# Performance work log

Measured on AMD Instinct MI355X. Metric: run time of the kernel, lower is better.

Reference implementation:

```python
import jax, jax.numpy as jnp
import numpy as np

DIM = 256
HEADS = 4
HEAD_DIM = DIM // HEADS          # 64
KEY_DIM = HEAD_DIM // 2          # 32 (attn_ratio=0.5)
HIDDEN = DIM + 2 * KEY_DIM * HEADS  # 512
B, H, W = 2, 64, 64
EPS = 1e-5


def _conv2d(x, w, groups=1, pad=0):
    return jax.lax.conv_general_dilated(
        x, w, window_strides=(1, 1), padding=[(pad, pad), (pad, pad)],
        dimension_numbers=('NCHW', 'OIHW', 'NCHW'), feature_group_count=groups)


def _bn(x, g, b, m, v):
    scale = g / jnp.sqrt(v + EPS)
    return x * scale[None, :, None, None] + (b - m * scale)[None, :, None, None]


def setup_inputs() -> dict:
    key = jax.random.key(0)
    ks = jax.random.split(key, 16)
    d = {
        'x': jax.random.normal(ks[0], (B, DIM, H, W), jnp.float32),
        'qkv_w': jax.random.normal(ks[1], (HIDDEN, DIM, 1, 1), jnp.float32) * 0.05,
        'qkv_g': jax.random.uniform(ks[2], (HIDDEN,), jnp.float32, 0.5, 1.5),
        'qkv_b': jax.random.normal(ks[3], (HIDDEN,), jnp.float32) * 0.1,
        'qkv_m': jax.random.normal(ks[4], (HIDDEN,), jnp.float32) * 0.1,
        'qkv_v': jax.random.uniform(ks[5], (HIDDEN,), jnp.float32, 0.5, 1.5),
        'proj_w': jax.random.normal(ks[6], (DIM, DIM, 1, 1), jnp.float32) * 0.05,
        'proj_g': jax.random.uniform(ks[7], (DIM,), jnp.float32, 0.5, 1.5),
        'proj_b': jax.random.normal(ks[8], (DIM,), jnp.float32) * 0.1,
        'proj_m': jax.random.normal(ks[9], (DIM,), jnp.float32) * 0.1,
        'proj_v': jax.random.uniform(ks[10], (DIM,), jnp.float32, 0.5, 1.5),
        'pe_w': jax.random.normal(ks[11], (DIM, 1, 3, 3), jnp.float32) * 0.1,
        'pe_g': jax.random.uniform(ks[12], (DIM,), jnp.float32, 0.5, 1.5),
        'pe_b': jax.random.normal(ks[13], (DIM,), jnp.float32) * 0.1,
        'pe_m': jax.random.normal(ks[14], (DIM,), jnp.float32) * 0.1,
        'pe_v': jax.random.uniform(ks[15], (DIM,), jnp.float32, 0.5, 1.5),
    }
    return d


def reference(x, qkv_w, qkv_g, qkv_b, qkv_m, qkv_v,
              proj_w, proj_g, proj_b, proj_m, proj_v,
              pe_w, pe_g, pe_b, pe_m, pe_v):
    b, c, h, w = x.shape
    n = h * w
    scale = KEY_DIM ** -0.5

    qkv = _bn(_conv2d(x, qkv_w), qkv_g, qkv_b, qkv_m, qkv_v)  # [b, hidden, h, w]
    qkv = qkv.reshape(b, HEADS, 2 * KEY_DIM + HEAD_DIM, n)
    q = qkv[:, :, :KEY_DIM]                       # [b, heads, key_dim, n]
    k = qkv[:, :, KEY_DIM:2 * KEY_DIM]            # [b, heads, key_dim, n]
    v = qkv[:, :, 2 * KEY_DIM:]                   # [b, heads, head_dim, n]

    # attn[b,h,i,j] = sum_d q[b,h,d,i] * k[b,h,d,j] * scale; softmax over j
    attn = jnp.einsum('bhdi,bhdj->bhij', q, k) * scale
    attn = jax.nn.softmax(attn, axis=-1)

    # y = v @ attn^T : out[b,h,d,i] = sum_j v[b,h,d,j] * attn[b,h,i,j]
    y = jnp.einsum('bhdj,bhij->bhdi', v, attn).reshape(b, c, h, w)

    pe = _bn(_conv2d(v.reshape(b, c, h, w), pe_w, groups=c, pad=1),
             pe_g, pe_b, pe_m, pe_v)
    y = y + pe
    return _bn(_conv2d(y, proj_w), proj_g, proj_b, proj_m, proj_v)
```

## Files before the change

kernel.cpp:

```cpp
#include <hip/hip_runtime.h>
#include <hip/hip_bf16.h>

#define NSP 4096
#define BEPS 1e-5f
#define JSPLIT 4
#define JCHUNK (NSP / JSPLIT)

using short8  = __attribute__((ext_vector_type(8))) short;
using half8   = __attribute__((ext_vector_type(8))) _Float16;
using f32x4   = __attribute__((ext_vector_type(4))) float;
using f32x16  = __attribute__((ext_vector_type(16))) float;

#define SCALE_LOG2E 0.2550348883f

__device__ __forceinline__ float b2f(unsigned short u) {
  return __uint_as_float(((unsigned)u) << 16);
}
__device__ __forceinline__ float b2f_lo(unsigned w) {
  return __uint_as_float(w << 16);
}
__device__ __forceinline__ float b2f_hi(unsigned w) {
  return __uint_as_float(w & 0xffff0000u);
}
__device__ __forceinline__ unsigned short f2b(float x) {
  unsigned u = __float_as_uint(x);
  u += 0x7fffu + ((u >> 16) & 1u);
  return (unsigned short)(u >> 16);
}
__device__ __forceinline__ unsigned pk_bf16(float a, float b) {
  return ((unsigned)f2b(b) << 16) | (unsigned)f2b(a);
}
__device__ __forceinline__ unsigned pk2u(float a, float b) {
  __hip_bfloat162 h = __float22bfloat162_rn(float2{a, b});
  unsigned r;
  __builtin_memcpy(&r, &h, sizeof(r));
  return r;
}
__device__ __forceinline__ unsigned short f2h(float x) {
  _Float16 h = (_Float16)x;
  unsigned short u;
  __builtin_memcpy(&u, &h, sizeof(u));
  return u;
}
__device__ __forceinline__ unsigned pk_h2(float a, float b) {
  return ((unsigned)f2h(b) << 16) | (unsigned)f2h(a);
}

__global__ __launch_bounds__(256) void cast_w_kernel(
    const float* __restrict__ qkv_w, const float* __restrict__ proj_w,
    unsigned short* __restrict__ wqb, unsigned short* __restrict__ wpb)
{
  const int i = blockIdx.x * 256 + threadIdx.x;
  if (i < 131072)       wqb[i] = f2h(qkv_w[i]);
  else                  wpb[i - 131072] = f2b(proj_w[i - 131072]);
}

__global__ __launch_bounds__(256) void transpose_x_kernel(
    const float* __restrict__ x, unsigned short* __restrict__ xT)
{
  const int n0 = blockIdx.x * 64, c0 = blockIdx.y * 64, b = blockIdx.z;
  __shared__ __align__(16) unsigned short tx[64][72];
  const int t = threadIdx.x;
  const int row = t >> 2;
  const int seg = t & 3;
  {
    const float* xp = x + ((size_t)(b * 256 + c0 + row)) * NSP + n0 + seg * 16;
    #pragma unroll
    for (int q4 = 0; q4 < 4; ++q4) {
      const float4 a = *reinterpret_cast<const float4*>(xp + q4 * 4);
      tx[seg * 16 + q4 * 4 + 0][row] = f2h(a.x);
      tx[seg * 16 + q4 * 4 + 1][row] = f2h(a.y);
      tx[seg * 16 + q4 * 4 + 2][row] = f2h(a.z);
      tx[seg * 16 + q4 * 4 + 3][row] = f2h(a.w);
    }
  }
  __syncthreads();
  const int nrow = t >> 2, ch = t & 3;
  unsigned short* op = xT + ((size_t)(b * NSP + n0 + nrow)) * 256 + c0 + ch * 16;
  *reinterpret_cast<float4*>(op)     = *reinterpret_cast<const float4*>(&tx[nrow][ch * 16]);
  *reinterpret_cast<float4*>(op + 8) = *reinterpret_cast<const float4*>(&tx[nrow][ch * 16 + 8]);
}

__global__ __launch_bounds__(256) void qkv_gemm_kernel(
    const unsigned short* __restrict__ xT, const unsigned short* __restrict__ wqb,
    const float* __restrict__ gg, const float* __restrict__ bb,
    const float* __restrict__ mm, const float* __restrict__ vv,
    unsigned short* __restrict__ qb, unsigned short* __restrict__ kb,
    unsigned short* __restrict__ vb)
{
  const int n0 = blockIdx.x * 128;
  const int cotile = blockIdx.y;
  const int b = blockIdx.z;
  const int co0 = cotile * 64;
  const int t = threadIdx.x;
  __shared__ __align__(16) unsigned short wt[64][136];
  __shared__ __align__(16) unsigned short xt[128][136];
  const int lane = t & 63, wave = t >> 6;
  const int m16 = lane & 15, quad = lane >> 4;

  f32x4 acc[8] = {};
  for (int kc = 0; kc < 2; ++kc) {
    if (kc) __syncthreads();
    {
      const unsigned short* wp = wqb + (size_t)(co0 + (t >> 2)) * 256 + kc * 128 + (t & 3) * 32;
      #pragma unroll
      for (int u = 0; u < 4; ++u)
        *reinterpret_cast<float4*>(&wt[t >> 2][(t & 3) * 32 + u * 8]) =
            *reinterpret_cast<const float4*>(wp + u * 8);
      const unsigned short* xp = xT + ((size_t)(b * NSP + n0 + (t >> 1))) * 256 + kc * 128 + (t & 1) * 64;
      #pragma unroll
      for (int u = 0; u < 8; ++u)
        *reinterpret_cast<float4*>(&xt[t >> 1][(t & 1) * 64 + u * 8]) =
            *reinterpret_cast<const float4*>(xp + u * 8);
    }
    __syncthreads();
    if ((cotile & 1) == 0) {
      #pragma unroll
      for (int ks = 0; ks < 4; ++ks) {
        const half8 af = *reinterpret_cast<const half8*>(&wt[wave * 16 + m16][ks * 32 + quad * 8]);
        #pragma unroll
        for (int nt = 0; nt < 8; ++nt) {
          const half8 bf = *reinterpret_cast<const half8*>(&xt[nt * 16 + m16][ks * 32 + quad * 8]);
          acc[nt] = __builtin_amdgcn_mfma_f32_16x16x32_f16(af, bf, acc[nt], 0, 0, 0);
        }
      }
    } else {
      #pragma unroll
      for (int ks = 0; ks < 4; ++ks) {
        const half8 bf = *reinterpret_cast<const half8*>(&wt[wave * 16 + m16][ks * 32 + quad * 8]);
        #pragma unroll
        for (int nt = 0; nt < 8; ++nt) {
          const half8 af = *reinterpret_cast<const half8*>(&xt[nt * 16 + m16][ks * 32 + quad * 8]);
          acc[nt] = __builtin_amdgcn_mfma_f32_16x16x32_f16(af, bf, acc[nt], 0, 0, 0);
        }
      }
    }
  }

  const int head = cotile >> 1;
  const int bh = b * 4 + head;
  if ((cotile & 1) == 0) {
    const int coh = wave * 16 + quad * 4;
    const bool isq = (coh < 32);
    const float fold = isq ? SCALE_LOG2E : 1.0f;
    float sc[4], bi[4];
    #pragma unroll
    for (int r = 0; r < 4; ++r) {
      const int c = co0 + coh + r;
      const float s0 = gg[c] * rsqrtf(vv[c] + BEPS);
      sc[r] = s0 * fold;
      bi[r] = (bb[c] - mm[c] * s0) * fold;
    }
    unsigned short* dst = isq ? qb : kb;
    const int d0 = coh & 31;
    #pragma unroll
    for (int nt = 0; nt < 8; ++nt) {
      const int i = n0 + nt * 16 + m16;
      uint2 pk2;
      pk2.x = pk_h2(acc[nt][0] * sc[0] + bi[0], acc[nt][1] * sc[1] + bi[1]);
      pk2.y = pk_h2(acc[nt][2] * sc[2] + bi[2], acc[nt][3] * sc[3] + bi[3]);
      *reinterpret_cast<uint2*>(dst + ((size_t)bh * NSP + i) * 32 + d0) = pk2;
    }
  } else {
    const int c = co0 + wave * 16 + m16;
    const float sc = gg[c] * rsqrtf(vv[c] + BEPS);
    const float bi = bb[c] - mm[c] * sc;
    const int d = wave * 16 + m16;
    #pragma unroll
    for (int nt = 0; nt < 8; ++nt) {
      const int j = n0 + nt * 16 + quad * 4;
      uint2 pk2;
      pk2.x = pk_bf16(acc[nt][0] * sc + bi, acc[nt][1] * sc + bi);
      pk2.y = pk_bf16(acc[nt][2] * sc + bi, acc[nt][3] * sc + bi);
      *reinterpret_cast<uint2*>(vb + ((size_t)(bh * 64 + d)) * NSP + j) = pk2;
    }
  }
}

__global__ __launch_bounds__(256, 4) void attn_kernel(
    const unsigned short* __restrict__ qb, const unsigned short* __restrict__ kb,
    const unsigned short* __restrict__ vb,
    unsigned short* __restrict__ Opart, float* __restrict__ lpart)
{
  const int i0    = blockIdx.x * 128;
  const int bh    = blockIdx.y;
  const int split = blockIdx.z;
  const int jbase = split * JCHUNK;
  const int t  = threadIdx.x;
  const int lane = t & 63, wave = t >> 6;
  const int l31 = lane & 31, hi = lane >> 5;

  __shared__ __align__(16) unsigned short qs[128][40];
  __shared__ __align__(16) unsigned short ks[64][40];
  __shared__ __align__(16) unsigned short vs[64][72];

  {
    const unsigned short* qp = qb + ((size_t)bh * NSP + i0) * 32;
    const int r = t >> 1, h = t & 1;
    *reinterpret_cast<float4*>(&qs[r][h * 16]) =
        *reinterpret_cast<const float4*>(qp + r * 32 + h * 16);
    *reinterpret_cast<float4*>(&qs[r][h * 16 + 8]) =
        *reinterpret_cast<const float4*>(qp + r * 32 + h * 16 + 8);
  }

  const int srow = t >> 2, schunk = t & 3;
  const unsigned short* kbase = kb + (size_t)bh * NSP * 32;
  const unsigned short* vbase = vb + (size_t)bh * 64 * NSP;

  float4 kreg, vreg0, vreg1;
  kreg  = *reinterpret_cast<const float4*>(kbase + (size_t)(jbase + srow) * 32 + schunk * 8);
  vreg0 = *reinterpret_cast<const float4*>(vbase + (size_t)srow * NSP + jbase + schunk * 16);
  vreg1 = *reinterpret_cast<const float4*>(vbase + (size_t)srow * NSP + jbase + schunk * 16 + 8);

  __syncthreads();
  half8 qfrag[2];
  qfrag[0] = *reinterpret_cast<const half8*>(&qs[wave * 32 + l31][hi * 8]);
  qfrag[1] = *reinterpret_cast<const half8*>(&qs[wave * 32 + l31][16 + hi * 8]);

  *reinterpret_cast<float4*>(&ks[srow][schunk * 8]) = kreg;
  *reinterpret_cast<float4*>(&vs[srow][schunk * 16]) = vreg0;
  *reinterpret_cast<float4*>(&vs[srow][schunk * 16 + 8]) = vreg1;
  __syncthreads();

  float rsum = 0.f;
  f32x16 oacc[2] = {};

  for (int jt0 = 0; jt0 < JCHUNK; jt0 += 64) {
    const bool more = (jt0 + 64) < JCHUNK;
    if (more) {
      const int jn = jbase + jt0 + 64;
      kreg  = *reinterpret_cast<const float4*>(kbase + (size_t)(jn + srow) * 32 + schunk * 8);
      vreg0 = *reinterpret_cast<const float4*>(vbase + (size_t)srow * NSP + jn + schunk * 16);
      vreg1 = *reinterpret_cast<const float4*>(vbase + (size_t)srow * NSP + jn + schunk * 16 + 8);
    }

    half8 kf[2][2];
    #pragma unroll
    for (int jt32 = 0; jt32 < 2; ++jt32) {
      kf[jt32][0] = *reinterpret_cast<const half8*>(&ks[jt32 * 32 + l31][hi * 8]);
      kf[jt32][1] = *reinterpret_cast<const half8*>(&ks[jt32 * 32 + l31][16 + hi * 8]);
    }

    #pragma unroll
    for (int jt32 = 0; jt32 < 2; ++jt32) {
      f32x16 sacc = {};
      sacc = __builtin_amdgcn_mfma_f32_32x32x16_f16(kf[jt32][0], qfrag[0], sacc, 0, 0, 0);
      sacc = __builtin_amdgcn_mfma_f32_32x32x16_f16(kf[jt32][1], qfrag[1], sacc, 0, 0, 0);

      unsigned pk[8];
      #pragma unroll
      for (int c = 0; c < 8; ++c) {
        const float p0 = __builtin_amdgcn_exp2f(sacc[2 * c]);
        const float p1 = __builtin_amdgcn_exp2f(sacc[2 * c + 1]);
        rsum += p0 + p1;
        pk[c] = pk2u(p0, p1);
      }

      #pragma unroll
      for (int kt = 0; kt < 2; ++kt) {
        const unsigned s_a0 = (unsigned)__shfl_xor((int)pk[4 * kt + 0], 32);
        const unsigned s_a1 = (unsigned)__shfl_xor((int)pk[4 * kt + 1], 32);
        const unsigned s_b0 = (unsigned)__shfl_xor((int)pk[4 * kt + 2], 32);
        const unsigned s_b1 = (unsigned)__shfl_xor((int)pk[4 * kt + 3], 32);
        uint4 aw;
        aw.x = hi ? s_b0 : pk[4 * kt + 0];
        aw.y = hi ? s_b1 : pk[4 * kt + 1];
        aw.z = hi ? pk[4 * kt + 2] : s_a0;
        aw.w = hi ? pk[4 * kt + 3] : s_a1;
        short8 af;
        __builtin_memcpy(&af, &aw, 16);
        #pragma unroll
        for (int dt = 0; dt < 2; ++dt) {
          const short8 vf = *reinterpret_cast<const short8*>(
              &vs[dt * 32 + l31][jt32 * 32 + kt * 16 + hi * 8]);
          oacc[dt] = __builtin_amdgcn_mfma_f32_32x32x16_bf16(af, vf, oacc[dt], 0, 0, 0);
        }
      }
    }

    if (more) {
      __syncthreads();
      *reinterpret_cast<float4*>(&ks[srow][schunk * 8]) = kreg;
      *reinterpret_cast<float4*>(&vs[srow][schunk * 16]) = vreg0;
      *reinterpret_cast<float4*>(&vs[srow][schunk * 16 + 8]) = vreg1;
      __syncthreads();
    }
  }

  {
    float rs = rsum;
    rs += __shfl_xor(rs, 32);
    if (hi == 0)
      lpart[((size_t)split * 8 + bh) * NSP + i0 + wave * 32 + l31] = rs;
  }

  #pragma unroll
  for (int dt = 0; dt < 2; ++dt) {
    const int d = dt * 32 + l31;
    #pragma unroll
    for (int R = 0; R < 4; ++R) {
      uint2 pk2;
      pk2.x = pk2u(oacc[dt][4 * R + 0], oacc[dt][4 * R + 1]);
      pk2.y = pk2u(oacc[dt][4 * R + 2], oacc[dt][4 * R + 3]);
      *reinterpret_cast<uint2*>(Opart +
          (((size_t)split * 8 + bh) * 64 + d) * NSP + i0 + wave * 32 + 8 * R + 4 * hi) = pk2;
    }
  }
}

__global__ __launch_bounds__(256) void fuse_kernel(
    const unsigned short* __restrict__ Opart, const float* __restrict__ lpart,
    const unsigned short* __restrict__ vb,
    const float* __restrict__ pw, const float* __restrict__ pg,
    const float* __restrict__ pb, const float* __restrict__ pm,
    const float* __restrict__ pv,
    unsigned short* __restrict__ yT)
{
  const int py = blockIdx.x;
  const int bh = blockIdx.y;
  const int b = bh >> 2, h = bh & 3;
  const int t = threadIdx.x;
  const int d = t >> 2, seg = t & 3;
  __shared__ float lsum[64];
  __shared__ __align__(16) unsigned short yt[64][72];

  if (t < 64) {
    float ls = 0.f;
    #pragma unroll
    for (int s = 0; s < JSPLIT; ++s)
      ls += lpart[((size_t)s * 8 + bh) * NSP + py * 64 + t];
    lsum[t] = ls;
  }
  __syncthreads();

  const int c = h * 64 + d;
  const int i0 = py * 64 + seg * 16;
  float os[16] = {};
  #pragma unroll
  for (int s = 0; s < JSPLIT; ++s) {
    const uint4* op = reinterpret_cast<const uint4*>(
        Opart + (((size_t)s * 8 + bh) * 64 + d) * NSP + i0);
    const uint4 a = op[0], e = op[1];
    os[0]  += b2f_lo(a.x); os[1]  += b2f_hi(a.x);
    os[2]  += b2f_lo(a.y); os[3]  += b2f_hi(a.y);
    os[4]  += b2f_lo(a.z); os[5]  += b2f_hi(a.z);
    os[6]  += b2f_lo(a.w); os[7]  += b2f_hi(a.w);
    os[8]  += b2f_lo(e.x); os[9]  += b2f_hi(e.x);
    os[10] += b2f_lo(e.y); os[11] += b2f_hi(e.y);
    os[12] += b2f_lo(e.z); os[13] += b2f_hi(e.z);
    os[14] += b2f_lo(e.w); os[15] += b2f_hi(e.w);
  }

  float w9[9];
  #pragma unroll
  for (int i = 0; i < 9; ++i) w9[i] = pw[c * 9 + i];
  const float sc = pg[c] * rsqrtf(pv[c] + BEPS);
  const float bi = pb[c] - pm[c] * sc;
  const unsigned short* vrow = vb + ((size_t)(bh * 64 + d)) * NSP;

  float conv[16] = {};
  #pragma unroll
  for (int dy = -1; dy <= 1; ++dy) {
    const int yy = py + dy;
    if (yy < 0 || yy > 63) continue;
    const unsigned short* vr = vrow + yy * 64 + seg * 16;
    float vals[18];
    const uint4 m0 = *reinterpret_cast<const uint4*>(vr);
    const uint4 m1 = *reinterpret_cast<const uint4*>(vr + 8);
    vals[1]  = b2f_lo(m0.x); vals[2]  = b2f_hi(m0.x);
    vals[3]  = b2f_lo(m0.y); vals[4]  = b2f_hi(m0.y);
    vals[5]  = b2f_lo(m0.z); vals[6]  = b2f_hi(m0.z);
    vals[7]  = b2f_lo(m0.w); vals[8]  = b2f_hi(m0.w);
    vals[9]  = b2f_lo(m1.x); vals[10] = b2f_hi(m1.x);
    vals[11] = b2f_lo(m1.y); vals[12] = b2f_hi(m1.y);
    vals[13] = b2f_lo(m1.z); vals[14] = b2f_hi(m1.z);
    vals[15] = b2f_lo(m1.w); vals[16] = b2f_hi(m1.w);
    vals[0]  = (seg > 0) ? b2f_hi(*reinterpret_cast<const unsigned*>(vr - 2)) : 0.f;
    vals[17] = (seg < 3) ? b2f_lo(*reinterpret_cast<const unsigned*>(vr + 16)) : 0.f;
    const float wr0 = w9[(dy + 1) * 3 + 0], wr1 = w9[(dy + 1) * 3 + 1], wr2 = w9[(dy + 1) * 3 + 2];
    #pragma unroll
    for (int u = 0; u < 16; ++u)
      conv[u] += vals[u] * wr0 + vals[u + 1] * wr1 + vals[u + 2] * wr2;
  }

  #pragma unroll
  for (int u = 0; u < 16; ++u) {
    const float yv = os[u] / lsum[seg * 16 + u] + conv[u] * sc + bi;
    yt[seg * 16 + u][d] = f2b(yv);
  }
  __syncthreads();

  const int prow = t >> 2, ch = t & 3;
  unsigned short* op = yT + ((size_t)(b * NSP + py * 64 + prow)) * 256 + h * 64 + ch * 16;
  *reinterpret_cast<float4*>(op)     = *reinterpret_cast<const float4*>(&yt[prow][ch * 16]);
  *reinterpret_cast<float4*>(op + 8) = *reinterpret_cast<const float4*>(&yt[prow][ch * 16 + 8]);
}

__global__ __launch_bounds__(256) void proj_gemm_kernel(
    const unsigned short* __restrict__ yT, const unsigned short* __restrict__ wpb,
    const float* __restrict__ gg, const float* __restrict__ bb,
    const float* __restrict__ mm, const float* __restrict__ vv,
    float* __restrict__ out)
{
  const int n0 = blockIdx.x * 128;
  const int co0 = blockIdx.y * 64;
  const int b = blockIdx.z;
  const int t = threadIdx.x;
  __shared__ __align__(16) unsigned short wt[64][136];
  __shared__ __align__(16) unsigned short yt[128][136];
  const int lane = t & 63, wave = t >> 6;
  const int m16 = lane & 15, quad = lane >> 4;

  f32x4 acc[8] = {};
  for (int kc = 0; kc < 2; ++kc) {
    if (kc) __syncthreads();
    {
      const unsigned short* wp = wpb + (size_t)(co0 + (t >> 2)) * 256 + kc * 128 + (t & 3) * 32;
      #pragma unroll
      for (int u = 0; u < 4; ++u)
        *reinterpret_cast<float4*>(&wt[t >> 2][(t & 3) * 32 + u * 8]) =
            *reinterpret_cast<const float4*>(wp + u * 8);
      const unsigned short* yp = yT + ((size_t)(b * NSP + n0 + (t >> 1))) * 256 + kc * 128 + (t & 1) * 64;
      #pragma unroll
      for (int u = 0; u < 8; ++u)
        *reinterpret_cast<float4*>(&yt[t >> 1][(t & 1) * 64 + u * 8]) =
            *reinterpret_cast<const float4*>(yp + u * 8);
    }
    __syncthreads();
    #pragma unroll
    for (int ks = 0; ks < 4; ++ks) {
      const short8 bf = *reinterpret_cast<const short8*>(&wt[wave * 16 + m16][ks * 32 + quad * 8]);
      #pragma unroll
      for (int nt = 0; nt < 8; ++nt) {
        const short8 af = *reinterpret_cast<const short8*>(&yt[nt * 16 + m16][ks * 32 + quad * 8]);
        acc[nt] = __builtin_amdgcn_mfma_f32_16x16x32_bf16(af, bf, acc[nt], 0, 0, 0);
      }
    }
  }

  const int c = co0 + wave * 16 + m16;
  const float sc = gg[c] * rsqrtf(vv[c] + BEPS);
  const float bi = bb[c] - mm[c] * sc;
  #pragma unroll
  for (int nt = 0; nt < 8; ++nt) {
    const int n = n0 + nt * 16 + quad * 4;
    float4 ov;
    ov.x = acc[nt][0] * sc + bi; ov.y = acc[nt][1] * sc + bi;
    ov.z = acc[nt][2] * sc + bi; ov.w = acc[nt][3] * sc + bi;
    *reinterpret_cast<float4*>(out + ((size_t)(b * 256 + c)) * NSP + n) = ov;
  }
}

extern "C" void kernel_launch(void* const* d_in, const int* in_sizes, int n_in,
                              void* d_out, int out_size, void* d_ws, size_t ws_size,
                              hipStream_t stream)
{
  const float* x      = (const float*)d_in[0];
  const float* qkv_w  = (const float*)d_in[1];
  const float* qkv_g  = (const float*)d_in[2];
  const float* qkv_b  = (const float*)d_in[3];
  const float* qkv_m  = (const float*)d_in[4];
  const float* qkv_v  = (const float*)d_in[5];
  const float* proj_w = (const float*)d_in[6];
  const float* proj_g = (const float*)d_in[7];
  const float* proj_b = (const float*)d_in[8];
  const float* proj_m = (const float*)d_in[9];
  const float* proj_v = (const float*)d_in[10];
  const float* pe_w   = (const float*)d_in[11];
  const float* pe_g   = (const float*)d_in[12];
  const float* pe_b   = (const float*)d_in[13];
  const float* pe_m   = (const float*)d_in[14];
  const float* pe_v   = (const float*)d_in[15];
  float* out = (float*)d_out;

  unsigned short* qb = (unsigned short*)d_ws;
  unsigned short* kb = qb + (size_t)8 * NSP * 32;
  unsigned short* vb = kb + (size_t)8 * NSP * 32;
  unsigned short* Opart = vb + (size_t)8 * 64 * NSP;
  float* lpart = (float*)(Opart + (size_t)JSPLIT * 8 * 64 * NSP);
  unsigned short* xT = (unsigned short*)(lpart + (size_t)JSPLIT * 8 * NSP);
  unsigned short* yT = xT + (size_t)2 * NSP * 256;
  unsigned short* wqb = yT + (size_t)2 * NSP * 256;
  unsigned short* wpb = wqb + (size_t)512 * 256;

  cast_w_kernel<<<dim3(768), 256, 0, stream>>>(qkv_w, proj_w, wqb, wpb);
  transpose_x_kernel<<<dim3(64, 4, 2), 256, 0, stream>>>(x, xT);
  qkv_gemm_kernel<<<dim3(32, 8, 2), 256, 0, stream>>>(xT, wqb, qkv_g, qkv_b, qkv_m, qkv_v,
                                                      qb, kb, vb);
  attn_kernel<<<dim3(32, 8, JSPLIT), 256, 0, stream>>>(qb, kb, vb, Opart, lpart);
  fuse_kernel<<<dim3(64, 8), 256, 0, stream>>>(Opart, lpart, vb,
                                               pe_w, pe_g, pe_b, pe_m, pe_v, yT);
  proj_gemm_kernel<<<dim3(32, 4, 2), 256, 0, stream>>>(yT, wpb, proj_g, proj_b, proj_m, proj_v,
                                                       out);
}
```

Before: 158.6 us.

## Fuse weight cast into transpose, drop attn shuffles, shrink proj tiles

Merges the weight-cast kernel into the x-transpose kernel as an extra grid slice, removing one launch. In attention, Q and K share LDS space, and V is stored with an interleaved layout so each lane's packed P values already match the MFMA operand order. This removes four cross-lane shuffles and selects per inner step. The fuse kernel multiplies by a precomputed reciprocal of the softmax sum instead of dividing. The projection GEMM uses 64-wide spatial tiles to double its block count, at the cost of reloading the weight tile more often.

```diff
diff --git a/kernel.cpp b/kernel.cpp
--- a/kernel.cpp
+++ b/kernel.cpp
@@ -46,21 +46,24 @@
   return ((unsigned)f2h(b) << 16) | (unsigned)f2h(a);
 }
 
-__global__ __launch_bounds__(256) void cast_w_kernel(
+__global__ __launch_bounds__(256) void transpose_x_kernel(
+    const float* __restrict__ x, unsigned short* __restrict__ xT,
     const float* __restrict__ qkv_w, const float* __restrict__ proj_w,
     unsigned short* __restrict__ wqb, unsigned short* __restrict__ wpb)
 {
-  const int i = blockIdx.x * 256 + threadIdx.x;
-  if (i < 131072)       wqb[i] = f2h(qkv_w[i]);
-  else                  wpb[i - 131072] = f2b(proj_w[i - 131072]);
-}
-
-__global__ __launch_bounds__(256) void transpose_x_kernel(
-    const float* __restrict__ x, unsigned short* __restrict__ xT)
-{
+  const int t = threadIdx.x;
+  if (blockIdx.z == 2) {
+    const int tid = (blockIdx.x * 4 + blockIdx.y) * 256 + t;
+    #pragma unroll
+    for (int u = 0; u < 3; ++u) {
+      const int i = tid + u * 65536;
+      if (i < 131072)  wqb[i] = f2h(qkv_w[i]);
+      else             wpb[i - 131072] = f2b(proj_w[i - 131072]);
+    }
+    return;
+  }
   const int n0 = blockIdx.x * 64, c0 = blockIdx.y * 64, b = blockIdx.z;
   __shared__ __align__(16) unsigned short tx[64][72];
-  const int t = threadIdx.x;
   const int row = t >> 2;
   const int seg = t & 3;
   {
@@ -190,9 +193,10 @@
   const int lane = t & 63, wave = t >> 6;
   const int l31 = lane & 31, hi = lane >> 5;
 
-  __shared__ __align__(16) unsigned short qs[128][40];
-  __shared__ __align__(16) unsigned short ks[64][40];
-  __shared__ __align__(16) unsigned short vs[64][72];
+  __shared__ __align__(16) unsigned short smem[7168];
+  unsigned short (*qs)[40] = (unsigned short(*)[40])smem;
+  unsigned short (*ks)[40] = (unsigned short(*)[40])smem;
+  unsigned short (*vs)[72] = (unsigned short(*)[72])(smem + 2560);
 
   {
     const unsigned short* qp = qb + ((size_t)bh * NSP + i0) * 32;
@@ -216,10 +220,18 @@
   half8 qfrag[2];
   qfrag[0] = *reinterpret_cast<const half8*>(&qs[wave * 32 + l31][hi * 8]);
   qfrag[1] = *reinterpret_cast<const half8*>(&qs[wave * 32 + l31][16 + hi * 8]);
+  __syncthreads();
 
   *reinterpret_cast<float4*>(&ks[srow][schunk * 8]) = kreg;
-  *reinterpret_cast<float4*>(&vs[srow][schunk * 16]) = vreg0;
-  *reinterpret_cast<float4*>(&vs[srow][schunk * 16 + 8]) = vreg1;
+  {
+    uint2* vd = reinterpret_cast<uint2*>(&vs[srow][schunk * 16]);
+    const uint2* v0 = reinterpret_cast<const uint2*>(&vreg0);
+    const uint2* v1 = reinterpret_cast<const uint2*>(&vreg1);
+    vd[0] = v0[0];
+    vd[1] = v1[0];
+    vd[2] = v0[1];
+    vd[3] = v1[1];
+  }
   __syncthreads();
 
   float rsum = 0.f;
@@ -258,15 +270,11 @@
 
       #pragma unroll
       for (int kt = 0; kt < 2; ++kt) {
-        const unsigned s_a0 = (unsigned)__shfl_xor((int)pk[4 * kt + 0], 32);
-        const unsigned s_a1 = (unsigned)__shfl_xor((int)pk[4 * kt + 1], 32);
-        const unsigned s_b0 = (unsigned)__shfl_xor((int)pk[4 * kt + 2], 32);
-        const unsigned s_b1 = (unsigned)__shfl_xor((int)pk[4 * kt + 3], 32);
         uint4 aw;
-        aw.x = hi ? s_b0 : pk[4 * kt + 0];
-        aw.y = hi ? s_b1 : pk[4 * kt + 1];
-        aw.z = hi ? pk[4 * kt + 2] : s_a0;
-        aw.w = hi ? pk[4 * kt + 3] : s_a1;
+        aw.x = pk[4 * kt + 0];
+        aw.y = pk[4 * kt + 1];
+        aw.z = pk[4 * kt + 2];
+        aw.w = pk[4 * kt + 3];
         short8 af;
         __builtin_memcpy(&af, &aw, 16);
         #pragma unroll
@@ -281,8 +289,13 @@
     if (more) {
       __syncthreads();
       *reinterpret_cast<float4*>(&ks[srow][schunk * 8]) = kreg;
-      *reinterpret_cast<float4*>(&vs[srow][schunk * 16]) = vreg0;
-      *reinterpret_cast<float4*>(&vs[srow][schunk * 16 + 8]) = vreg1;
+      uint2* vd = reinterpret_cast<uint2*>(&vs[srow][schunk * 16]);
+      const uint2* v0 = reinterpret_cast<const uint2*>(&vreg0);
+      const uint2* v1 = reinterpret_cast<const uint2*>(&vreg1);
+      vd[0] = v0[0];
+      vd[1] = v1[0];
+      vd[2] = v0[1];
+      vd[3] = v1[1];
       __syncthreads();
     }
   }
@@ -329,7 +342,7 @@
     #pragma unroll
     for (int s = 0; s < JSPLIT; ++s)
       ls += lpart[((size_t)s * 8 + bh) * NSP + py * 64 + t];
-    lsum[t] = ls;
+    lsum[t] = 1.0f / ls;
   }
   __syncthreads();
 
@@ -385,7 +398,7 @@
 
   #pragma unroll
   for (int u = 0; u < 16; ++u) {
-    const float yv = os[u] / lsum[seg * 16 + u] + conv[u] * sc + bi;
+    const float yv = os[u] * lsum[seg * 16 + u] + conv[u] * sc + bi;
     yt[seg * 16 + u][d] = f2b(yv);
   }
   __syncthreads();
@@ -402,16 +415,16 @@
     const float* __restrict__ mm, const float* __restrict__ vv,
     float* __restrict__ out)
 {
-  const int n0 = blockIdx.x * 128;
+  const int n0 = blockIdx.x * 64;
   const int co0 = blockIdx.y * 64;
   const int b = blockIdx.z;
   const int t = threadIdx.x;
   __shared__ __align__(16) unsigned short wt[64][136];
-  __shared__ __align__(16) unsigned short yt[128][136];
+  __shared__ __align__(16) unsigned short yt[64][136];
   const int lane = t & 63, wave = t >> 6;
   const int m16 = lane & 15, quad = lane >> 4;
 
-  f32x4 acc[8] = {};
+  f32x4 acc[4] = {};
   for (int kc = 0; kc < 2; ++kc) {
     if (kc) __syncthreads();
     {
@@ -420,10 +433,10 @@
       for (int u = 0; u < 4; ++u)
         *reinterpret_cast<float4*>(&wt[t >> 2][(t & 3) * 32 + u * 8]) =
             *reinterpret_cast<const float4*>(wp + u * 8);
-      const unsigned short* yp = yT + ((size_t)(b * NSP + n0 + (t >> 1))) * 256 + kc * 128 + (t & 1) * 64;
-      #pragma unroll
-      for (int u = 0; u < 8; ++u)
-        *reinterpret_cast<float4*>(&yt[t >> 1][(t & 1) * 64 + u * 8]) =
+      const unsigned short* yp = yT + ((size_t)(b * NSP + n0 + (t >> 2))) * 256 + kc * 128 + (t & 3) * 32;
+      #pragma unroll
+      for (int u = 0; u < 4; ++u)
+        *reinterpret_cast<float4*>(&yt[t >> 2][(t & 3) * 32 + u * 8]) =
             *reinterpret_cast<const float4*>(yp + u * 8);
     }
     __syncthreads();
@@ -431,7 +444,7 @@
     for (int ks = 0; ks < 4; ++ks) {
       const short8 bf = *reinterpret_cast<const short8*>(&wt[wave * 16 + m16][ks * 32 + quad * 8]);
       #pragma unroll
-      for (int nt = 0; nt < 8; ++nt) {
+      for (int nt = 0; nt < 4; ++nt) {
         const short8 af = *reinterpret_cast<const short8*>(&yt[nt * 16 + m16][ks * 32 + quad * 8]);
         acc[nt] = __builtin_amdgcn_mfma_f32_16x16x32_bf16(af, bf, acc[nt], 0, 0, 0);
       }
@@ -442,7 +455,7 @@
   const float sc = gg[c] * rsqrtf(vv[c] + BEPS);
   const float bi = bb[c] - mm[c] * sc;
   #pragma unroll
-  for (int nt = 0; nt < 8; ++nt) {
+  for (int nt = 0; nt < 4; ++nt) {
     const int n = n0 + nt * 16 + quad * 4;
     float4 ov;
     ov.x = acc[nt][0] * sc + bi; ov.y = acc[nt][1] * sc + bi;
@@ -483,13 +496,12 @@
   unsigned short* wqb = yT + (size_t)2 * NSP * 256;
   unsigned short* wpb = wqb + (size_t)512 * 256;
 
-  cast_w_kernel<<<dim3(768), 256, 0, stream>>>(qkv_w, proj_w, wqb, wpb);
-  transpose_x_kernel<<<dim3(64, 4, 2), 256, 0, stream>>>(x, xT);
+  transpose_x_kernel<<<dim3(64, 4, 3), 256, 0, stream>>>(x, xT, qkv_w, proj_w, wqb, wpb);
   qkv_gemm_kernel<<<dim3(32, 8, 2), 256, 0, stream>>>(xT, wqb, qkv_g, qkv_b, qkv_m, qkv_v,
                                                       qb, kb, vb);
   attn_kernel<<<dim3(32, 8, JSPLIT), 256, 0, stream>>>(qb, kb, vb, Opart, lpart);
   fuse_kernel<<<dim3(64, 8), 256, 0, stream>>>(Opart, lpart, vb,
                                                pe_w, pe_g, pe_b, pe_m, pe_v, yT);
-  proj_gemm_kernel<<<dim3(32, 4, 2), 256, 0, stream>>>(yT, wpb, proj_g, proj_b, proj_m, proj_v,
+  proj_gemm_kernel<<<dim3(64, 4, 2), 256, 0, stream>>>(yT, wpb, proj_g, proj_b, proj_m, proj_v,
                                                        out);
 }
```

Result: faster. 149.5 us (-5.7%).
